# Performance work log

Hardware: AMD Instinct MI355X
Metric: run time of the kernel (lower is better)

The kernel has to match this reference:

```python
import jax, jax.numpy as jnp
import numpy as np

# Qwen3-VL-MoE text experts (training path): token permute -> grouped GEMM
# (gate_up) -> SwiGLU -> grouped GEMM (down) -> token unpermute + prob combine.
# Routing is generated perfectly balanced (each expert receives exactly M/E
# expanded tokens) so the grouped GEMM over the sorted token buffer is exactly
# a batched matmul over E contiguous groups -- same math as npu_grouped_matmul.

E, H, D, T, K = 32, 2048, 768, 4096, 8  # experts, hidden, moe_intermediate, tokens, top_k
M = T * K                                # expanded rows


def setup_inputs() -> dict:
    key = jax.random.key(0)
    k1, k2, k3, k4, k5 = jax.random.split(key, 5)
    hidden_states = jax.random.normal(k1, (T, H), dtype=jnp.float32)
    routing_weights = jax.nn.softmax(jax.random.normal(k2, (T, E), dtype=jnp.float32), axis=-1)
    # balanced expert assignment: each expert id appears exactly M // E times
    flat = jnp.tile(jnp.arange(E, dtype=jnp.int32), M // E)
    router_indices = jax.random.permutation(k3, flat).reshape(T, K)
    gate_up_proj = jax.random.normal(k4, (E, H, 2 * D), dtype=jnp.float32) * 0.02
    down_proj = jax.random.normal(k5, (E, D, H), dtype=jnp.float32) * 0.02
    return {
        "hidden_states": hidden_states,
        "routing_weights": routing_weights,
        "router_indices": router_indices,
        "gate_up_proj": gate_up_proj,
        "down_proj": down_proj,
    }


def reference(hidden_states, routing_weights, router_indices, gate_up_proj, down_proj):
    n_tok, hid = hidden_states.shape
    n_exp = gate_up_proj.shape[0]
    top_k = router_indices.shape[1]
    n_rows = n_tok * top_k
    grp = n_rows // n_exp  # balanced group size

    # --- npu_moe_token_permute: sort expanded (token, slot) rows by expert id
    flat_experts = router_indices.reshape(-1)            # (M,)
    order = jnp.argsort(flat_experts)                    # stable sort by expert
    permuted = hidden_states[order // top_k]             # (M, H)

    # --- grouped GEMM #1 (gate_up): balanced groups -> batched matmul
    xg = permuted.reshape(n_exp, grp, hid)               # (E, g, H)
    gate_up = jnp.einsum('egh,ehd->egd', xg, gate_up_proj)  # (E, g, 2D)

    # --- npu_swiglu(dim=-1): silu(first half) * second half
    gate, up = jnp.split(gate_up, 2, axis=-1)
    act = jax.nn.silu(gate) * up                         # (E, g, D)

    # --- grouped GEMM #2 (down)
    out = jnp.einsum('egd,edh->egh', act, down_proj).reshape(n_rows, hid)

    # --- npu_moe_token_unpermute: invert permutation, combine with probs
    inv = jnp.argsort(order)
    expanded = out[inv].reshape(n_tok, top_k, hid)       # (T, K, H)
    probs = jnp.take_along_axis(routing_weights, router_indices, axis=1)  # (T, K)
    return jnp.einsum('tkh,tk->th', expanded, probs)     # (T, H)
```

## Files before the change

### kernel.cpp

```cpp
#include <hip/hip_runtime.h>
#include <hip/hip_bf16.h>
#include <cstdint>


#define E_   32
#define H_   2048
#define D_   768
#define T_   4096
#define K_   8
#define M_   (T_ * K_)
#define G_   (M_ / E_)
#define GU2  (2 * D_)

typedef unsigned short u16;
typedef short bf16x8 __attribute__((ext_vector_type(8)));
typedef float f32x4 __attribute__((ext_vector_type(4)));
typedef unsigned short u16x2 __attribute__((ext_vector_type(2)));
typedef unsigned short u16x8 __attribute__((ext_vector_type(8)));

__device__ __forceinline__ u16 f2bf(float f) {
  unsigned u = __float_as_uint(f);
  u += 0x7FFFu + ((u >> 16) & 1u);
  return (u16)(u >> 16);
}
__device__ __forceinline__ float bf2f(u16 v) {
  return __uint_as_float(((unsigned)v) << 16);
}

#define GLOAD16(g, l) __builtin_amdgcn_global_load_lds(                        \
    (const __attribute__((address_space(1))) void*)(g),                        \
    (__attribute__((address_space(3))) void*)(l), 16, 0, 0)

#define VM8()   asm volatile("s_waitcnt vmcnt(8)" ::: "memory")
#define VM4()   asm volatile("s_waitcnt vmcnt(4)" ::: "memory")
#define VM0()   asm volatile("s_waitcnt vmcnt(0)" ::: "memory")
#define LGKM0() asm volatile("s_waitcnt lgkmcnt(0)" ::: "memory")
#define SCHB()  __builtin_amdgcn_sched_barrier(0)
#define BAR()   __builtin_amdgcn_s_barrier()

__global__ __launch_bounds__(256) void cvt_hidden(const float* __restrict__ in,
                                                  u16* __restrict__ out) {
  const int i = blockIdx.x * 256 + threadIdx.x;
  const float4 v = ((const float4*)in)[i];
  u16x2 a; a.x = f2bf(v.x); a.y = f2bf(v.y);
  u16x2 b; b.x = f2bf(v.z); b.y = f2bf(v.w);
  *(u16x2*)&out[(size_t)i * 4]     = a;
  *(u16x2*)&out[(size_t)i * 4 + 2] = b;
}

__global__ __launch_bounds__(256) void transpose_cvt(const float* __restrict__ in,
                                                     u16* __restrict__ out,
                                                     int R, int C, int mode) {
  __shared__ u16 tl[64 * 72];
  const int b = blockIdx.z;
  const int c0 = blockIdx.x * 64, r0 = blockIdx.y * 64;
  const int tid = threadIdx.x;
  const float* ip = in + ((size_t)b * R + r0) * C + c0;
  const int rr4 = tid >> 4;
  const int cc4 = (tid & 15) * 4;
#pragma unroll
  for (int p = 0; p < 4; ++p) {
    const int r = p * 16 + rr4;
    const float4 v = *(const float4*)&ip[(size_t)r * C + cc4];
    tl[(cc4 + 0) * 72 + r] = f2bf(v.x);
    tl[(cc4 + 1) * 72 + r] = f2bf(v.y);
    tl[(cc4 + 2) * 72 + r] = f2bf(v.z);
    tl[(cc4 + 3) * 72 + r] = f2bf(v.w);
  }
  __syncthreads();
  const int rs = (tid & 7) * 8;
#pragma unroll
  for (int q = 0; q < 2; ++q) {
    const int c = q * 32 + (tid >> 3);
    const int gc = c0 + c;
    int rr;
    if (mode == 1) {
      const int j = (gc < D_) ? gc : (gc - D_);
      rr = (j >> 4) * 32 + ((gc < D_) ? 0 : 16) + (j & 15);
    } else {
      rr = gc;
    }
    const u16x8 v = *(const u16x8*)&tl[c * 72 + rs];
    *(u16x8*)&out[((size_t)b * C + rr) * R + r0 + rs] = v;
  }
}

__global__ __launch_bounds__(256) void build_perm_fast(const int* __restrict__ ridx,
                                                       int* __restrict__ perm,
                                                       int* __restrict__ gcnt) {
  __shared__ int lc[E_];
  __shared__ int lb[E_];
  const int tid = threadIdx.x;
  if (tid < E_) lc[tid] = 0;
  __syncthreads();
  const int i = blockIdx.x * 256 + tid;
  const int e = ridx[i];
  const int p = atomicAdd(&lc[e], 1);
  __syncthreads();
  if (tid < E_) lb[tid] = atomicAdd(&gcnt[tid], lc[tid]);
  __syncthreads();
  perm[e * G_ + lb[e] + p] = i;
}

__global__ __launch_bounds__(512, 2) void gemm1_swiglu(
    const u16* __restrict__ hid, const u16* __restrict__ gup,
    const int* __restrict__ perm, u16* __restrict__ act) {
  __shared__ u16 As[4][8192];
  __shared__ u16 Bs[4][8192];
  const int NT = H_ / 32;

  const int nwg = 6 * 4 * E_;
  const int wid = (blockIdx.x % 8) * (nwg / 8) + blockIdx.x / 8;
  const int e = wid / 24;
  const int mb = (wid / 6) % 4;
  const int nb = wid % 6;

  const int tid = threadIdx.x;
  const int lane = tid & 63, w = tid >> 6;
  const int wr = w >> 2, wc = w & 3;

  const int srow = tid >> 2, schunk = tid & 3;
  const u16* pA[2]; const u16* pB[2];
#pragma unroll
  for (int q = 0; q < 2; ++q) {
    const int r = q * 128 + srow;
    const int cg = (schunk ^ ((r >> 1) & 3)) * 8;
    const int token = perm[e * G_ + mb * 256 + r] >> 3;
    pA[q] = hid + (size_t)token * H_ + cg;
    pB[q] = gup + ((size_t)e * GU2 + nb * 256 + r) * H_ + cg;
  }

  int aoff[8], boff[4];
  {
    const int l15 = lane & 15, hk = lane >> 4;
#pragma unroll
    for (int m = 0; m < 8; ++m) {
      const int rA = wr * 128 + m * 16 + l15;
      aoff[m] = rA * 32 + ((hk ^ ((rA >> 1) & 3)) * 8);
    }
#pragma unroll
    for (int n = 0; n < 4; ++n) {
      const int rB = wc * 64 + n * 16 + l15;
      boff[n] = rB * 32 + ((hk ^ ((rB >> 1) & 3)) * 8);
    }
  }

  f32x4 acc[8][4];
#pragma unroll
  for (int m = 0; m < 8; ++m)
#pragma unroll
    for (int n = 0; n < 4; ++n) acc[m][n] = (f32x4){0.f, 0.f, 0.f, 0.f};

  GLOAD16(pA[0], &As[0][tid * 8]);      GLOAD16(pA[1], &As[0][4096 + tid * 8]);
  GLOAD16(pB[0], &Bs[0][tid * 8]);      GLOAD16(pB[1], &Bs[0][4096 + tid * 8]);
  GLOAD16(pA[0] + 32, &As[1][tid * 8]); GLOAD16(pA[1] + 32, &As[1][4096 + tid * 8]);
  GLOAD16(pB[0] + 32, &Bs[1][tid * 8]); GLOAD16(pB[1] + 32, &Bs[1][4096 + tid * 8]);
  GLOAD16(pA[0] + 64, &As[2][tid * 8]); GLOAD16(pA[1] + 64, &As[2][4096 + tid * 8]);
  GLOAD16(pB[0] + 64, &Bs[2][tid * 8]); GLOAD16(pB[1] + 64, &Bs[2][4096 + tid * 8]);
  VM8(); BAR(); SCHB();

#pragma unroll 4
  for (int t = 0; t < NT; ++t) {
    const int slot = t & 3, ts = (t + 3) & 3;
    const bool st = (t + 3) < NT;
    const u16* Ab = As[slot]; const u16* Bb = Bs[slot];
    bf16x8 av[4], bv[4];
#pragma unroll
    for (int n = 0; n < 4; ++n) bv[n] = *(const bf16x8*)&Bb[boff[n]];
#pragma unroll
    for (int m = 0; m < 4; ++m) av[m] = *(const bf16x8*)&Ab[aoff[m]];
    if (st) {
      GLOAD16(pA[0] + (t + 3) * 32, &As[ts][tid * 8]);
      GLOAD16(pA[1] + (t + 3) * 32, &As[ts][4096 + tid * 8]);
    }
    SCHB(); BAR(); LGKM0(); SCHB();
    __builtin_amdgcn_s_setprio(1);
#pragma unroll
    for (int m = 0; m < 4; ++m)
#pragma unroll
      for (int n = 0; n < 4; ++n)
        acc[m][n] = __builtin_amdgcn_mfma_f32_16x16x32_bf16(av[m], bv[n],
                                                            acc[m][n], 0, 0, 0);
    __builtin_amdgcn_s_setprio(0);
    SCHB(); BAR();
#pragma unroll
    for (int m = 0; m < 4; ++m) av[m] = *(const bf16x8*)&Ab[aoff[m + 4]];
    if (st) {
      GLOAD16(pB[0] + (t + 3) * 32, &Bs[ts][tid * 8]);
      GLOAD16(pB[1] + (t + 3) * 32, &Bs[ts][4096 + tid * 8]);
    }
    SCHB(); BAR(); LGKM0(); SCHB();
    __builtin_amdgcn_s_setprio(1);
#pragma unroll
    for (int m = 0; m < 4; ++m)
#pragma unroll
      for (int n = 0; n < 4; ++n)
        acc[m + 4][n] = __builtin_amdgcn_mfma_f32_16x16x32_bf16(av[m], bv[n],
                                                                acc[m + 4][n], 0, 0, 0);
    __builtin_amdgcn_s_setprio(0);
    SCHB();
    if (t + 3 < NT)      { VM8(); }
    else if (t + 2 < NT) { VM4(); }
    else                 { VM0(); }
    BAR();
  }

  const int lrow = (lane >> 4) * 4, lcol = lane & 15;
#pragma unroll
  for (int m = 0; m < 8; ++m)
#pragma unroll
    for (int p = 0; p < 2; ++p)
#pragma unroll
      for (int r = 0; r < 4; ++r) {
        const float g = acc[m][2 * p][r];
        const float u = acc[m][2 * p + 1][r];
        const float a_ = g / (1.f + __expf(-g)) * u;
        const int row = mb * 256 + wr * 128 + m * 16 + lrow + r;
        const int dcol = (nb * 8 + wc * 2 + p) * 16 + lcol;
        act[((size_t)e * G_ + row) * D_ + dcol] = f2bf(a_);
      }
}

__global__ __launch_bounds__(512, 2) void gemm2_scatter(
    const u16* __restrict__ act, const u16* __restrict__ dwn,
    const int* __restrict__ perm, u16* __restrict__ expo) {
  __shared__ u16 As[4][8192];
  __shared__ u16 Bs[4][8192];
  const int NT = D_ / 32;

  const int nwg = 8 * 4 * E_;
  const int wid = (blockIdx.x % 8) * (nwg / 8) + blockIdx.x / 8;
  const int e = wid / 32;
  const int mb = (wid / 8) % 4;
  const int nb = wid % 8;

  const int tid = threadIdx.x;
  const int lane = tid & 63, w = tid >> 6;
  const int wr = w >> 2, wc = w & 3;

  const int srow = tid >> 2, schunk = tid & 3;
  const u16* pA[2]; const u16* pB[2];
#pragma unroll
  for (int q = 0; q < 2; ++q) {
    const int r = q * 128 + srow;
    const int cg = (schunk ^ ((r >> 1) & 3)) * 8;
    pA[q] = act + ((size_t)e * G_ + mb * 256 + r) * D_ + cg;
    pB[q] = dwn + ((size_t)e * H_ + nb * 256 + r) * D_ + cg;
  }

  int aoff[8], boff[4];
  {
    const int l15 = lane & 15, hk = lane >> 4;
#pragma unroll
    for (int m = 0; m < 8; ++m) {
      const int rA = wr * 128 + m * 16 + l15;
      aoff[m] = rA * 32 + ((hk ^ ((rA >> 1) & 3)) * 8);
    }
#pragma unroll
    for (int n = 0; n < 4; ++n) {
      const int rB = wc * 64 + n * 16 + l15;
      boff[n] = rB * 32 + ((hk ^ ((rB >> 1) & 3)) * 8);
    }
  }

  f32x4 acc[8][4];
#pragma unroll
  for (int m = 0; m < 8; ++m)
#pragma unroll
    for (int n = 0; n < 4; ++n) acc[m][n] = (f32x4){0.f, 0.f, 0.f, 0.f};

  GLOAD16(pA[0], &As[0][tid * 8]);      GLOAD16(pA[1], &As[0][4096 + tid * 8]);
  GLOAD16(pB[0], &Bs[0][tid * 8]);      GLOAD16(pB[1], &Bs[0][4096 + tid * 8]);
  GLOAD16(pA[0] + 32, &As[1][tid * 8]); GLOAD16(pA[1] + 32, &As[1][4096 + tid * 8]);
  GLOAD16(pB[0] + 32, &Bs[1][tid * 8]); GLOAD16(pB[1] + 32, &Bs[1][4096 + tid * 8]);
  GLOAD16(pA[0] + 64, &As[2][tid * 8]); GLOAD16(pA[1] + 64, &As[2][4096 + tid * 8]);
  GLOAD16(pB[0] + 64, &Bs[2][tid * 8]); GLOAD16(pB[1] + 64, &Bs[2][4096 + tid * 8]);
  VM8(); BAR(); SCHB();

#pragma unroll 4
  for (int t = 0; t < NT; ++t) {
    const int slot = t & 3, ts = (t + 3) & 3;
    const bool st = (t + 3) < NT;
    const u16* Ab = As[slot]; const u16* Bb = Bs[slot];
    bf16x8 av[4], bv[4];
#pragma unroll
    for (int n = 0; n < 4; ++n) bv[n] = *(const bf16x8*)&Bb[boff[n]];
#pragma unroll
    for (int m = 0; m < 4; ++m) av[m] = *(const bf16x8*)&Ab[aoff[m]];
    if (st) {
      GLOAD16(pA[0] + (t + 3) * 32, &As[ts][tid * 8]);
      GLOAD16(pA[1] + (t + 3) * 32, &As[ts][4096 + tid * 8]);
    }
    SCHB(); BAR(); LGKM0(); SCHB();
    __builtin_amdgcn_s_setprio(1);
#pragma unroll
    for (int m = 0; m < 4; ++m)
#pragma unroll
      for (int n = 0; n < 4; ++n)
        acc[m][n] = __builtin_amdgcn_mfma_f32_16x16x32_bf16(av[m], bv[n],
                                                            acc[m][n], 0, 0, 0);
    __builtin_amdgcn_s_setprio(0);
    SCHB(); BAR();
#pragma unroll
    for (int m = 0; m < 4; ++m) av[m] = *(const bf16x8*)&Ab[aoff[m + 4]];
    if (st) {
      GLOAD16(pB[0] + (t + 3) * 32, &Bs[ts][tid * 8]);
      GLOAD16(pB[1] + (t + 3) * 32, &Bs[ts][4096 + tid * 8]);
    }
    SCHB(); BAR(); LGKM0(); SCHB();
    __builtin_amdgcn_s_setprio(1);
#pragma unroll
    for (int m = 0; m < 4; ++m)
#pragma unroll
      for (int n = 0; n < 4; ++n)
        acc[m + 4][n] = __builtin_amdgcn_mfma_f32_16x16x32_bf16(av[m], bv[n],
                                                                acc[m + 4][n], 0, 0, 0);
    __builtin_amdgcn_s_setprio(0);
    SCHB();
    if (t + 3 < NT)      { VM8(); }
    else if (t + 2 < NT) { VM4(); }
    else                 { VM0(); }
    BAR();
  }

  const int lrow = (lane >> 4) * 4, lcol = lane & 15;
#pragma unroll
  for (int m = 0; m < 8; ++m)
#pragma unroll
    for (int r = 0; r < 4; ++r) {
      const int dst = e * G_ + mb * 256 + wr * 128 + m * 16 + lrow + r;
      const int src = perm[dst];
      u16* orow = expo + (size_t)src * H_ + nb * 256 + wc * 64;
#pragma unroll
      for (int n = 0; n < 4; ++n)
        orow[n * 16 + lcol] = f2bf(acc[m][n][r]);
    }
}

__global__ __launch_bounds__(256) void combine(const u16* __restrict__ expo,
                                               const int* __restrict__ ridx,
                                               const float* __restrict__ rw,
                                               float* __restrict__ out) {
  __shared__ float pr[K_];
  const int t = blockIdx.x;
  if (threadIdx.x < K_)
    pr[threadIdx.x] = rw[t * E_ + ridx[t * K_ + threadIdx.x]];
  __syncthreads();
  const int h0 = threadIdx.x * 8;
  float r[8] = {0.f, 0.f, 0.f, 0.f, 0.f, 0.f, 0.f, 0.f};
#pragma unroll
  for (int k = 0; k < K_; ++k) {
    const float p = pr[k];
    const u16x8 v = *(const u16x8*)&expo[((size_t)(t * K_ + k)) * H_ + h0];
#pragma unroll
    for (int j = 0; j < 8; ++j) r[j] += p * bf2f(v[j]);
  }
  float4 o0 = {r[0], r[1], r[2], r[3]};
  float4 o1 = {r[4], r[5], r[6], r[7]};
  *(float4*)&out[(size_t)t * H_ + h0]     = o0;
  *(float4*)&out[(size_t)t * H_ + h0 + 4] = o1;
}

extern "C" void kernel_launch(void* const* d_in, const int* in_sizes, int n_in,
                              void* d_out, int out_size, void* d_ws, size_t ws_size,
                              hipStream_t stream) {
  const float* hidden = (const float*)d_in[0];
  const float* rw     = (const float*)d_in[1];
  const int*   ridx   = (const int*)d_in[2];
  const float* gup_f  = (const float*)d_in[3];
  const float* dwn_f  = (const float*)d_in[4];
  float* out = (float*)d_out;

  char* ws = (char*)d_ws;
  size_t off = 0;
  auto alloc = [&](size_t bytes) -> void* {
    void* p = ws + off;
    off += (bytes + 255) & ~(size_t)255;
    return p;
  };
  u16*   hid_bf = (u16*)alloc((size_t)T_ * H_ * 2);
  u16*   gup_t  = (u16*)alloc((size_t)E_ * GU2 * H_ * 2);
  u16*   dwn_t  = (u16*)alloc((size_t)E_ * H_ * D_ * 2);
  u16*   act    = (u16*)alloc((size_t)M_ * D_ * 2);
  u16*   expo   = (u16*)alloc((size_t)M_ * H_ * 2);
  int*   perm   = (int*)alloc((size_t)M_ * 4);
  int*   gcnt   = (int*)alloc((size_t)E_ * 4);
  if (off > ws_size) return;

  hipMemsetAsync(gcnt, 0, E_ * sizeof(int), stream);
  cvt_hidden<<<(T_ * H_ / 4) / 256, 256, 0, stream>>>(hidden, hid_bf);
  transpose_cvt<<<dim3(GU2 / 64, H_ / 64, E_), 256, 0, stream>>>(gup_f, gup_t, H_, GU2, 1);
  transpose_cvt<<<dim3(H_ / 64, D_ / 64, E_), 256, 0, stream>>>(dwn_f, dwn_t, D_, H_, 0);
  build_perm_fast<<<M_ / 256, 256, 0, stream>>>(ridx, perm, gcnt);
  gemm1_swiglu<<<6 * 4 * E_, 512, 0, stream>>>(hid_bf, gup_t, perm, act);
  gemm2_scatter<<<8 * 4 * E_, 512, 0, stream>>>(act, dwn_t, perm, expo);
  combine<<<T_, 256, 0, stream>>>(expo, ridx, rw, out);
}
```

Before: 541.2 us.

## Fuse weight fp32-to-bf16 transpose into GEMM B-tile loads via register staging

Drops the two standalone transpose_cvt kernels and instead has each GEMM block read fp32 weights directly from global memory into registers, convert them to bf16 and write them transposed into a padded LDS tile (pitch 40). The B operand pipeline moves from a 4-deep async global-to-LDS prefetch to a register-staged double buffer, and the A prefetch depth drops from 3 to 2. This removes a full read-convert-write pass over the weights and its workspace traffic. In exchange, every M-block re-reads and re-converts the fp32 weights (twice the bytes per load), adds VALU and LDS store work inside the main loop, and shortens latency hiding.

```diff
diff --git a/kernel.cpp b/kernel.cpp
--- a/kernel.cpp
+++ b/kernel.cpp
@@ -11,11 +11,13 @@
 #define M_   (T_ * K_)
 #define G_   (M_ / E_)
 #define GU2  (2 * D_)
+#define BPITCH 40
 
 typedef unsigned short u16;
 typedef short bf16x8 __attribute__((ext_vector_type(8)));
 typedef float f32x4 __attribute__((ext_vector_type(4)));
 typedef unsigned short u16x2 __attribute__((ext_vector_type(2)));
+typedef unsigned short u16x4 __attribute__((ext_vector_type(4)));
 typedef unsigned short u16x8 __attribute__((ext_vector_type(8)));
 
 __device__ __forceinline__ u16 f2bf(float f) {
@@ -31,8 +33,7 @@
     (const __attribute__((address_space(1))) void*)(g),                        \
     (__attribute__((address_space(3))) void*)(l), 16, 0, 0)
 
-#define VM8()   asm volatile("s_waitcnt vmcnt(8)" ::: "memory")
-#define VM4()   asm volatile("s_waitcnt vmcnt(4)" ::: "memory")
+#define VM6()   asm volatile("s_waitcnt vmcnt(6)" ::: "memory")
 #define VM0()   asm volatile("s_waitcnt vmcnt(0)" ::: "memory")
 #define LGKM0() asm volatile("s_waitcnt lgkmcnt(0)" ::: "memory")
 #define SCHB()  __builtin_amdgcn_sched_barrier(0)
@@ -46,43 +47,6 @@
   u16x2 b; b.x = f2bf(v.z); b.y = f2bf(v.w);
   *(u16x2*)&out[(size_t)i * 4]     = a;
   *(u16x2*)&out[(size_t)i * 4 + 2] = b;
-}
-
-__global__ __launch_bounds__(256) void transpose_cvt(const float* __restrict__ in,
-                                                     u16* __restrict__ out,
-                                                     int R, int C, int mode) {
-  __shared__ u16 tl[64 * 72];
-  const int b = blockIdx.z;
-  const int c0 = blockIdx.x * 64, r0 = blockIdx.y * 64;
-  const int tid = threadIdx.x;
-  const float* ip = in + ((size_t)b * R + r0) * C + c0;
-  const int rr4 = tid >> 4;
-  const int cc4 = (tid & 15) * 4;
-#pragma unroll
-  for (int p = 0; p < 4; ++p) {
-    const int r = p * 16 + rr4;
-    const float4 v = *(const float4*)&ip[(size_t)r * C + cc4];
-    tl[(cc4 + 0) * 72 + r] = f2bf(v.x);
-    tl[(cc4 + 1) * 72 + r] = f2bf(v.y);
-    tl[(cc4 + 2) * 72 + r] = f2bf(v.z);
-    tl[(cc4 + 3) * 72 + r] = f2bf(v.w);
-  }
-  __syncthreads();
-  const int rs = (tid & 7) * 8;
-#pragma unroll
-  for (int q = 0; q < 2; ++q) {
-    const int c = q * 32 + (tid >> 3);
-    const int gc = c0 + c;
-    int rr;
-    if (mode == 1) {
-      const int j = (gc < D_) ? gc : (gc - D_);
-      rr = (j >> 4) * 32 + ((gc < D_) ? 0 : 16) + (j & 15);
-    } else {
-      rr = gc;
-    }
-    const u16x8 v = *(const u16x8*)&tl[c * 72 + rs];
-    *(u16x8*)&out[((size_t)b * C + rr) * R + r0 + rs] = v;
-  }
 }
 
 __global__ __launch_bounds__(256) void build_perm_fast(const int* __restrict__ ridx,
@@ -103,10 +67,10 @@
 }
 
 __global__ __launch_bounds__(512, 2) void gemm1_swiglu(
-    const u16* __restrict__ hid, const u16* __restrict__ gup,
+    const u16* __restrict__ hid, const float* __restrict__ gup,
     const int* __restrict__ perm, u16* __restrict__ act) {
   __shared__ u16 As[4][8192];
-  __shared__ u16 Bs[4][8192];
+  __shared__ u16 Bs[2][256 * BPITCH];
   const int NT = H_ / 32;
 
   const int nwg = 6 * 4 * E_;
@@ -120,15 +84,24 @@
   const int wr = w >> 2, wc = w & 3;
 
   const int srow = tid >> 2, schunk = tid & 3;
-  const u16* pA[2]; const u16* pB[2];
+  const u16* pA[2];
 #pragma unroll
   for (int q = 0; q < 2; ++q) {
     const int r = q * 128 + srow;
     const int cg = (schunk ^ ((r >> 1) & 3)) * 8;
     const int token = perm[e * G_ + mb * 256 + r] >> 3;
     pA[q] = hid + (size_t)token * H_ + cg;
-    pB[q] = gup + ((size_t)e * GU2 + nb * 256 + r) * H_ + cg;
-  }
+  }
+
+  const int rt = tid >> 8;
+  const int u  = tid & 255;
+  const int hq = u & 7;
+  const int d4 = u >> 3;
+  const int dloc = d4 * 4;
+  const int h0 = hq * 4;
+  const int gc = rt * D_ + nb * 128 + dloc;
+  const int rb = (dloc >> 4) * 32 + rt * 16 + (dloc & 15);
+  const float* bsA = gup + ((size_t)e * H_ + h0) * GU2 + gc;
 
   int aoff[8], boff[4];
   {
@@ -141,7 +114,7 @@
 #pragma unroll
     for (int n = 0; n < 4; ++n) {
       const int rB = wc * 64 + n * 16 + l15;
-      boff[n] = rB * 32 + ((hk ^ ((rB >> 1) & 3)) * 8);
+      boff[n] = rB * BPITCH + hk * 8;
     }
   }
 
@@ -151,27 +124,43 @@
 #pragma unroll
     for (int n = 0; n < 4; ++n) acc[m][n] = (f32x4){0.f, 0.f, 0.f, 0.f};
 
+  f32x4 Lcur[4], Lnxt[4];
   GLOAD16(pA[0], &As[0][tid * 8]);      GLOAD16(pA[1], &As[0][4096 + tid * 8]);
-  GLOAD16(pB[0], &Bs[0][tid * 8]);      GLOAD16(pB[1], &Bs[0][4096 + tid * 8]);
+  SCHB();
+#pragma unroll
+  for (int j = 0; j < 4; ++j) Lcur[j] = *(const f32x4*)(bsA + (size_t)j * GU2);
+  SCHB();
   GLOAD16(pA[0] + 32, &As[1][tid * 8]); GLOAD16(pA[1] + 32, &As[1][4096 + tid * 8]);
-  GLOAD16(pB[0] + 32, &Bs[1][tid * 8]); GLOAD16(pB[1] + 32, &Bs[1][4096 + tid * 8]);
-  GLOAD16(pA[0] + 64, &As[2][tid * 8]); GLOAD16(pA[1] + 64, &As[2][4096 + tid * 8]);
-  GLOAD16(pB[0] + 64, &Bs[2][tid * 8]); GLOAD16(pB[1] + 64, &Bs[2][4096 + tid * 8]);
-  VM8(); BAR(); SCHB();
-
-#pragma unroll 4
+  SCHB();
+#pragma unroll
+  for (int j = 0; j < 4; ++j) Lnxt[j] = *(const f32x4*)(bsA + (size_t)(32 + j) * GU2);
+  SCHB();
+  VM6();
+#pragma unroll
+  for (int i = 0; i < 4; ++i) {
+    const int r = rb + i;
+    u16x4 v;
+    v[0] = f2bf(Lcur[0][i]); v[1] = f2bf(Lcur[1][i]);
+    v[2] = f2bf(Lcur[2][i]); v[3] = f2bf(Lcur[3][i]);
+    *(u16x4*)&Bs[0][r * BPITCH + h0] = v;
+  }
+#pragma unroll
+  for (int j = 0; j < 4; ++j) Lcur[j] = Lnxt[j];
+  LGKM0(); BAR(); SCHB();
+
+#pragma unroll 2
   for (int t = 0; t < NT; ++t) {
-    const int slot = t & 3, ts = (t + 3) & 3;
-    const bool st = (t + 3) < NT;
-    const u16* Ab = As[slot]; const u16* Bb = Bs[slot];
+    const int slot = t & 3, ts = (t + 2) & 3;
+    const bool st2 = (t + 2) < NT, st1 = (t + 1) < NT;
+    const u16* Ab = As[slot]; const u16* Bb = Bs[t & 1];
     bf16x8 av[4], bv[4];
 #pragma unroll
     for (int n = 0; n < 4; ++n) bv[n] = *(const bf16x8*)&Bb[boff[n]];
 #pragma unroll
     for (int m = 0; m < 4; ++m) av[m] = *(const bf16x8*)&Ab[aoff[m]];
-    if (st) {
-      GLOAD16(pA[0] + (t + 3) * 32, &As[ts][tid * 8]);
-      GLOAD16(pA[1] + (t + 3) * 32, &As[ts][4096 + tid * 8]);
+    if (st2) {
+      GLOAD16(pA[0] + (t + 2) * 32, &As[ts][tid * 8]);
+      GLOAD16(pA[1] + (t + 2) * 32, &As[ts][4096 + tid * 8]);
     }
     SCHB(); BAR(); LGKM0(); SCHB();
     __builtin_amdgcn_s_setprio(1);
@@ -185,9 +174,11 @@
     SCHB(); BAR();
 #pragma unroll
     for (int m = 0; m < 4; ++m) av[m] = *(const bf16x8*)&Ab[aoff[m + 4]];
-    if (st) {
-      GLOAD16(pB[0] + (t + 3) * 32, &Bs[ts][tid * 8]);
-      GLOAD16(pB[1] + (t + 3) * 32, &Bs[ts][4096 + tid * 8]);
+    f32x4 Lnew[4];
+    if (st2) {
+#pragma unroll
+      for (int j = 0; j < 4; ++j)
+        Lnew[j] = *(const f32x4*)(bsA + (size_t)((t + 2) * 32 + j) * GU2);
     }
     SCHB(); BAR(); LGKM0(); SCHB();
     __builtin_amdgcn_s_setprio(1);
@@ -199,10 +190,22 @@
                                                                 acc[m + 4][n], 0, 0, 0);
     __builtin_amdgcn_s_setprio(0);
     SCHB();
-    if (t + 3 < NT)      { VM8(); }
-    else if (t + 2 < NT) { VM4(); }
-    else                 { VM0(); }
-    BAR();
+    if (st2)      { VM6(); }
+    else if (st1) { VM0(); }
+    if (st1) {
+#pragma unroll
+      for (int i = 0; i < 4; ++i) {
+        const int r = rb + i;
+        u16x4 v;
+        v[0] = f2bf(Lcur[0][i]); v[1] = f2bf(Lcur[1][i]);
+        v[2] = f2bf(Lcur[2][i]); v[3] = f2bf(Lcur[3][i]);
+        *(u16x4*)&Bs[(t + 1) & 1][r * BPITCH + h0] = v;
+      }
+#pragma unroll
+      for (int j = 0; j < 4; ++j) Lcur[j] = Lnew[j];
+      LGKM0();
+    }
+    BAR(); SCHB();
   }
 
   const int lrow = (lane >> 4) * 4, lcol = lane & 15;
@@ -213,8 +216,8 @@
 #pragma unroll
       for (int r = 0; r < 4; ++r) {
         const float g = acc[m][2 * p][r];
-        const float u = acc[m][2 * p + 1][r];
-        const float a_ = g / (1.f + __expf(-g)) * u;
+        const float uu = acc[m][2 * p + 1][r];
+        const float a_ = g / (1.f + __expf(-g)) * uu;
         const int row = mb * 256 + wr * 128 + m * 16 + lrow + r;
         const int dcol = (nb * 8 + wc * 2 + p) * 16 + lcol;
         act[((size_t)e * G_ + row) * D_ + dcol] = f2bf(a_);
@@ -222,10 +225,10 @@
 }
 
 __global__ __launch_bounds__(512, 2) void gemm2_scatter(
-    const u16* __restrict__ act, const u16* __restrict__ dwn,
+    const u16* __restrict__ act, const float* __restrict__ dwn,
     const int* __restrict__ perm, u16* __restrict__ expo) {
   __shared__ u16 As[4][8192];
-  __shared__ u16 Bs[4][8192];
+  __shared__ u16 Bs[2][256 * BPITCH];
   const int NT = D_ / 32;
 
   const int nwg = 8 * 4 * E_;
@@ -239,14 +242,19 @@
   const int wr = w >> 2, wc = w & 3;
 
   const int srow = tid >> 2, schunk = tid & 3;
-  const u16* pA[2]; const u16* pB[2];
+  const u16* pA[2];
 #pragma unroll
   for (int q = 0; q < 2; ++q) {
     const int r = q * 128 + srow;
     const int cg = (schunk ^ ((r >> 1) & 3)) * 8;
     pA[q] = act + ((size_t)e * G_ + mb * 256 + r) * D_ + cg;
-    pB[q] = dwn + ((size_t)e * H_ + nb * 256 + r) * D_ + cg;
-  }
+  }
+
+  const int kq  = tid & 7;
+  const int h64 = (tid >> 3) & 63;
+  const int d0  = kq * 4;
+  const int rb  = h64 * 4;
+  const float* bsB = dwn + ((size_t)e * D_ + d0) * H_ + nb * 256 + rb;
 
   int aoff[8], boff[4];
   {
@@ -259,7 +267,7 @@
 #pragma unroll
     for (int n = 0; n < 4; ++n) {
       const int rB = wc * 64 + n * 16 + l15;
-      boff[n] = rB * 32 + ((hk ^ ((rB >> 1) & 3)) * 8);
+      boff[n] = rB * BPITCH + hk * 8;
     }
   }
 
@@ -269,27 +277,43 @@
 #pragma unroll
     for (int n = 0; n < 4; ++n) acc[m][n] = (f32x4){0.f, 0.f, 0.f, 0.f};
 
+  f32x4 Lcur[4], Lnxt[4];
   GLOAD16(pA[0], &As[0][tid * 8]);      GLOAD16(pA[1], &As[0][4096 + tid * 8]);
-  GLOAD16(pB[0], &Bs[0][tid * 8]);      GLOAD16(pB[1], &Bs[0][4096 + tid * 8]);
+  SCHB();
+#pragma unroll
+  for (int j = 0; j < 4; ++j) Lcur[j] = *(const f32x4*)(bsB + (size_t)j * H_);
+  SCHB();
   GLOAD16(pA[0] + 32, &As[1][tid * 8]); GLOAD16(pA[1] + 32, &As[1][4096 + tid * 8]);
-  GLOAD16(pB[0] + 32, &Bs[1][tid * 8]); GLOAD16(pB[1] + 32, &Bs[1][4096 + tid * 8]);
-  GLOAD16(pA[0] + 64, &As[2][tid * 8]); GLOAD16(pA[1] + 64, &As[2][4096 + tid * 8]);
-  GLOAD16(pB[0] + 64, &Bs[2][tid * 8]); GLOAD16(pB[1] + 64, &Bs[2][4096 + tid * 8]);
-  VM8(); BAR(); SCHB();
-
-#pragma unroll 4
+  SCHB();
+#pragma unroll
+  for (int j = 0; j < 4; ++j) Lnxt[j] = *(const f32x4*)(bsB + (size_t)(32 + j) * H_);
+  SCHB();
+  VM6();
+#pragma unroll
+  for (int i = 0; i < 4; ++i) {
+    const int r = rb + i;
+    u16x4 v;
+    v[0] = f2bf(Lcur[0][i]); v[1] = f2bf(Lcur[1][i]);
+    v[2] = f2bf(Lcur[2][i]); v[3] = f2bf(Lcur[3][i]);
+    *(u16x4*)&Bs[0][r * BPITCH + d0] = v;
+  }
+#pragma unroll
+  for (int j = 0; j < 4; ++j) Lcur[j] = Lnxt[j];
+  LGKM0(); BAR(); SCHB();
+
+#pragma unroll 2
   for (int t = 0; t < NT; ++t) {
-    const int slot = t & 3, ts = (t + 3) & 3;
-    const bool st = (t + 3) < NT;
-    const u16* Ab = As[slot]; const u16* Bb = Bs[slot];
+    const int slot = t & 3, ts = (t + 2) & 3;
+    const bool st2 = (t + 2) < NT, st1 = (t + 1) < NT;
+    const u16* Ab = As[slot]; const u16* Bb = Bs[t & 1];
     bf16x8 av[4], bv[4];
 #pragma unroll
     for (int n = 0; n < 4; ++n) bv[n] = *(const bf16x8*)&Bb[boff[n]];
 #pragma unroll
     for (int m = 0; m < 4; ++m) av[m] = *(const bf16x8*)&Ab[aoff[m]];
-    if (st) {
-      GLOAD16(pA[0] + (t + 3) * 32, &As[ts][tid * 8]);
-      GLOAD16(pA[1] + (t + 3) * 32, &As[ts][4096 + tid * 8]);
+    if (st2) {
+      GLOAD16(pA[0] + (t + 2) * 32, &As[ts][tid * 8]);
+      GLOAD16(pA[1] + (t + 2) * 32, &As[ts][4096 + tid * 8]);
     }
     SCHB(); BAR(); LGKM0(); SCHB();
     __builtin_amdgcn_s_setprio(1);
@@ -303,9 +327,11 @@
     SCHB(); BAR();
 #pragma unroll
     for (int m = 0; m < 4; ++m) av[m] = *(const bf16x8*)&Ab[aoff[m + 4]];
-    if (st) {
-      GLOAD16(pB[0] + (t + 3) * 32, &Bs[ts][tid * 8]);
-      GLOAD16(pB[1] + (t + 3) * 32, &Bs[ts][4096 + tid * 8]);
+    f32x4 Lnew[4];
+    if (st2) {
+#pragma unroll
+      for (int j = 0; j < 4; ++j)
+        Lnew[j] = *(const f32x4*)(bsB + (size_t)((t + 2) * 32 + j) * H_);
     }
     SCHB(); BAR(); LGKM0(); SCHB();
     __builtin_amdgcn_s_setprio(1);
@@ -317,10 +343,22 @@
                                                                 acc[m + 4][n], 0, 0, 0);
     __builtin_amdgcn_s_setprio(0);
     SCHB();
-    if (t + 3 < NT)      { VM8(); }
-    else if (t + 2 < NT) { VM4(); }
-    else                 { VM0(); }
-    BAR();
+    if (st2)      { VM6(); }
+    else if (st1) { VM0(); }
+    if (st1) {
+#pragma unroll
+      for (int i = 0; i < 4; ++i) {
+        const int r = rb + i;
+        u16x4 v;
+        v[0] = f2bf(Lcur[0][i]); v[1] = f2bf(Lcur[1][i]);
+        v[2] = f2bf(Lcur[2][i]); v[3] = f2bf(Lcur[3][i]);
+        *(u16x4*)&Bs[(t + 1) & 1][r * BPITCH + d0] = v;
+      }
+#pragma unroll
+      for (int j = 0; j < 4; ++j) Lcur[j] = Lnew[j];
+      LGKM0();
+    }
+    BAR(); SCHB();
   }
 
   const int lrow = (lane >> 4) * 4, lcol = lane & 15;
@@ -379,8 +417,6 @@
     return p;
   };
   u16*   hid_bf = (u16*)alloc((size_t)T_ * H_ * 2);
-  u16*   gup_t  = (u16*)alloc((size_t)E_ * GU2 * H_ * 2);
-  u16*   dwn_t  = (u16*)alloc((size_t)E_ * H_ * D_ * 2);
   u16*   act    = (u16*)alloc((size_t)M_ * D_ * 2);
   u16*   expo   = (u16*)alloc((size_t)M_ * H_ * 2);
   int*   perm   = (int*)alloc((size_t)M_ * 4);
@@ -389,10 +425,8 @@
 
   hipMemsetAsync(gcnt, 0, E_ * sizeof(int), stream);
   cvt_hidden<<<(T_ * H_ / 4) / 256, 256, 0, stream>>>(hidden, hid_bf);
-  transpose_cvt<<<dim3(GU2 / 64, H_ / 64, E_), 256, 0, stream>>>(gup_f, gup_t, H_, GU2, 1);
-  transpose_cvt<<<dim3(H_ / 64, D_ / 64, E_), 256, 0, stream>>>(dwn_f, dwn_t, D_, H_, 0);
   build_perm_fast<<<M_ / 256, 256, 0, stream>>>(ridx, perm, gcnt);
-  gemm1_swiglu<<<6 * 4 * E_, 512, 0, stream>>>(hid_bf, gup_t, perm, act);
-  gemm2_scatter<<<8 * 4 * E_, 512, 0, stream>>>(act, dwn_t, perm, expo);
+  gemm1_swiglu<<<6 * 4 * E_, 512, 0, stream>>>(hid_bf, gup_f, perm, act);
+  gemm2_scatter<<<8 * 4 * E_, 512, 0, stream>>>(act, dwn_f, perm, expo);
   combine<<<T_, 256, 0, stream>>>(expo, ridx, rw, out);
 }
```

Result: slower. 594.4 us (+9.8%).
